# Performance work log

Hardware: AMD Instinct MI355X
Metric: run time of the kernel (lower is better)

Reference implementation:

```python
import jax, jax.numpy as jnp
import numpy as np

N, I, R, A, O, HEADS, HW, KS = 16, 128, 256, 256, 256, 8, 24, 3
HC = A // HEADS  # head channels
DN = ('NCHW', 'OIHW', 'NCHW')


def _conv(x, w, padding):
    return jax.lax.conv_general_dilated(x, w, (1, 1), padding, dimension_numbers=DN)


def setup_inputs() -> dict:
    key = jax.random.key(0)
    ks = jax.random.split(key, 16)
    g = lambda k, shape, fan: jax.random.normal(k, shape, jnp.float32) * (fan ** -0.5)
    return {
        'x': jax.random.normal(ks[0], (N, I, HW, HW), jnp.float32),
        'h0': jax.random.normal(ks[1], (N, R, HW, HW), jnp.float32) * 0.1,
        'c0': jax.random.normal(ks[2], (N, R, HW, HW), jnp.float32) * 0.1,
        'w_in': g(ks[3], (R, I, 1, 1), I),
        'b_in': jnp.zeros((R,), jnp.float32),
        'wq_x': g(ks[4], (A, R, KS, KS), R * KS * KS * 2 * HC),
        'wq_h': g(ks[5], (A, R, KS, KS), R * KS * KS * 2 * HC),
        'wk_x': g(ks[6], (A, R, KS, KS), R * KS * KS),
        'wk_h': g(ks[7], (A, R, KS, KS), R * KS * KS),
        'wv_x': g(ks[8], (A, R, KS, KS), R * KS * KS * 2),
        'wv_h': g(ks[9], (A, R, KS, KS), R * KS * KS * 2),
        'bv': jnp.zeros((A,), jnp.float32),
        'wg_a': g(ks[10], (4 * R, A, 1, 1), A * 3),
        'bg': jnp.zeros((4 * R,), jnp.float32),
        'wg_x': g(ks[11], (4 * R, R, KS, KS), R * KS * KS * 3),
        'wg_h': g(ks[12], (4 * R, R, KS, KS), R * KS * KS * 3),
        'w_out': g(ks[13], (O, R, 1, 1), R),
        'b_out': jnp.zeros((O,), jnp.float32),
    }


def reference(x, h0, c0, w_in, b_in, wq_x, wq_h, wk_x, wk_h, wv_x, wv_h, bv,
              wg_a, bg, wg_x, wg_h, w_out, b_out):
    # input accumulation (1x1 conv per input, summed; single input here)
    xin = _conv(x, w_in, 'VALID') + b_in[None, :, None, None]  # [N,R,H,W]
    # q: SAME-padded 3x3 convs of x and h (Accumulate = sum)
    q = _conv(xin, wq_x, 'SAME') + _conv(h0, wq_h, 'SAME')      # [N,A,H,W]
    # k, v: VALID 3x3 convs -> spatially reduced key/value positions
    k = _conv(xin, wk_x, 'VALID') + _conv(h0, wk_h, 'VALID')    # [N,A,H-2,W-2]
    v = _conv(xin, wv_x, 'VALID') + _conv(h0, wv_h, 'VALID') + bv[None, :, None, None]
    Q = HW * HW
    D = (HW - KS + 1) * (HW - KS + 1)
    qh = q.reshape(N, HEADS, HC, Q)
    kh = k.reshape(N, HEADS, HC, D)
    vh = v.reshape(N, HEADS, HC, D)
    w = jax.nn.softmax(jnp.einsum('ngcq,ngcd->ngqd', qh, kh), axis=-1)  # [N,G,Q,D]
    a = jnp.einsum('ngcd,ngqd->ngcq', vh, w).reshape(N, A, HW, HW)
    # fused i,f,g,o gate projections: 1x1 conv on a + 3x3 SAME convs on x and h
    gates = (_conv(a, wg_a, 'VALID') + bg[None, :, None, None]
             + _conv(xin, wg_x, 'SAME') + _conv(h0, wg_h, 'SAME'))      # [N,4R,H,W]
    i, f, gg, o = jnp.split(gates, 4, axis=1)
    c = jax.nn.sigmoid(f) * c0 + jax.nn.sigmoid(i) * jnp.tanh(gg)
    h = jax.nn.sigmoid(o) * jnp.tanh(c)
    return _conv(h, w_out, 'VALID') + b_out[None, :, None, None]
```

## Files before the change

### kernel.cpp

```cpp
#include <hip/hip_runtime.h>
#include <cstddef>

constexpr int kN  = 16;
constexpr int kI  = 128;
constexpr int kHW = 24;
constexpr int kQ  = 576;
constexpr int kD  = 484;
constexpr int kDP = 512;
constexpr int kPP = 676;

constexpr int kKT1 = 144;
constexpr int kKT2 = 8;
constexpr int kKT3 = 8;

constexpr size_t H_XPAD   = 0;
constexpr size_t H_HPAD   = 2768896;
constexpr size_t H_APACK1 = 5537792;
constexpr size_t H_APACK2 = 13795328;
constexpr size_t H_APACK3 = 14057472;
constexpr size_t H_A16    = 14123008;
constexpr size_t H_H16    = 16482304;
constexpr size_t H_Q16C   = 18841600;
constexpr size_t H_KT16   = 21200896;
constexpr size_t H_VC16   = 23298048;
constexpr size_t HALF_ELEMS = 25395200;
constexpr size_t HALF_BYTES = HALF_ELEMS * 2;
constexpr size_t F_G = 0;

using half4    = __attribute__((ext_vector_type(4))) _Float16;
using half8    = __attribute__((ext_vector_type(8))) _Float16;
using floatx16 = __attribute__((ext_vector_type(16))) float;

__device__ __forceinline__ float sigm(float x) { return 1.0f / (1.0f + __expf(-x)); }
__device__ __forceinline__ float tanh_f(float x) {
    float e = __expf(2.0f * fabsf(x));
    float r = 1.0f - 2.0f / (e + 1.0f);
    return copysignf(r, x);
}

__device__ __forceinline__ half8 LD8(const _Float16* p) { return *(const half8*)p; }
__device__ __forceinline__ void ST8(_Float16* p, half8 v) { *(half8*)p = v; }

__global__ void pack1_kernel(const float* __restrict__ wq_x, const float* __restrict__ wq_h,
                             const float* __restrict__ wk_x, const float* __restrict__ wk_h,
                             const float* __restrict__ wv_x, const float* __restrict__ wv_h,
                             const float* __restrict__ wg_x, const float* __restrict__ wg_h,
                             _Float16* __restrict__ dst) {
    int pidx = blockIdx.x * 256 + threadIdx.x;
    int j = pidx & 7, row = (pidx >> 3) & 127, hl = (pidx >> 10) & 1, kk = (pidx >> 11) & 1;
    int tile = pidx >> 12;
    int mt = tile / kKT1, kt = tile - mt * kKT1;
    int m = mt * 128 + row;
    int k = kt * 32 + kk * 16 + hl * 8 + j;
    int srcs = (k >= 2304) ? 1 : 0;
    int r = k - srcs * 2304;
    int tap = r >> 8, ic = r & 255;
    const float *s1, *s2; int mm;
    if (m < 256)      { s1 = wq_x; s2 = wq_h; mm = m; }
    else if (m < 512) { s1 = wk_x; s2 = wk_h; mm = m - 256; }
    else if (m < 768) { s1 = wv_x; s2 = wv_h; mm = m - 512; }
    else              { s1 = wg_x; s2 = wg_h; mm = m - 768; }
    const float* sp = srcs ? s2 : s1;
    dst[pidx] = (_Float16)sp[(size_t)mm * 2304 + ic * 9 + tap];
}

__global__ void pack_flat_kernel(const float* __restrict__ src, _Float16* __restrict__ dst,
                                 int Ktot, int Ktiles) {
    int pidx = blockIdx.x * 256 + threadIdx.x;
    int j = pidx & 7, row = (pidx >> 3) & 127, hl = (pidx >> 10) & 1, kk = (pidx >> 11) & 1;
    int tile = pidx >> 12;
    int mt = tile / Ktiles, kt = tile - mt * Ktiles;
    int m = mt * 128 + row;
    int k = kt * 32 + kk * 16 + hl * 8 + j;
    dst[pidx] = (_Float16)src[(size_t)m * Ktot + k];
}

__global__ void pad_nhwc_kernel(const float* __restrict__ src, _Float16* __restrict__ dst) {
    __shared__ float tile[32][65];
    int pxt = blockIdx.x, ict = blockIdx.y, n = blockIdx.z;
    int tid = threadIdx.x;
    {
        int icl = tid >> 6, pxl = tid & 63;
        #pragma unroll
        for (int rep = 0; rep < 8; ++rep) {
            int ic = ict * 32 + rep * 4 + icl;
            tile[rep * 4 + icl][pxl] = src[((size_t)n * 256 + ic) * kQ + pxt * 64 + pxl];
        }
    }
    __syncthreads();
    {
        int icl = tid & 31, pxl0 = tid >> 5;
        #pragma unroll
        for (int rep = 0; rep < 8; ++rep) {
            int pxl = rep * 8 + pxl0;
            int px = pxt * 64 + pxl;
            int y = px / kHW, x = px - y * kHW;
            dst[((size_t)n * kPP + (size_t)(y + 1) * 26 + (x + 1)) * 256 + ict * 32 + icl] =
                (_Float16)tile[icl][pxl];
        }
    }
}

__global__ void conv1x1_pad_kernel(const float* __restrict__ x, const float* __restrict__ w,
                                   const float* __restrict__ b, _Float16* __restrict__ out) {
    int px = blockIdx.x * 64 + threadIdx.x;
    int n = blockIdx.z;
    int oc0 = __builtin_amdgcn_readfirstlane(blockIdx.y * 16 + threadIdx.y * 4);
    const float* ip = x + (size_t)n * kI * kQ + px;
    float acc[4] = {0.f, 0.f, 0.f, 0.f};
    #pragma unroll 4
    for (int ic = 0; ic < kI; ++ic) {
        float xv = ip[(size_t)ic * kQ];
        #pragma unroll
        for (int j = 0; j < 4; ++j) acc[j] = fmaf(xv, w[(size_t)(oc0 + j) * kI + ic], acc[j]);
    }
    int y = px / kHW, xc = px - y * kHW;
    _Float16* op = out + ((size_t)n * kPP + (size_t)(y + 1) * 26 + (xc + 1)) * 256 + oc0;
    #pragma unroll
    for (int j = 0; j < 4; ++j) op[j] = (_Float16)(acc[j] + b[oc0 + j]);
}

template<int BMODE, int EMODE>
__global__ __launch_bounds__(256)
void gemm_kernel(const _Float16* __restrict__ Apack,
                 const _Float16* __restrict__ B1, const _Float16* __restrict__ B2,
                 _Float16* __restrict__ q16, _Float16* __restrict__ k16,
                 _Float16* __restrict__ v16, float* __restrict__ pf,
                 const float* __restrict__ bias, int Ktiles, int Ktot) {
    __shared__ _Float16 Bs[2][2048];
    const int tid = threadIdx.x;
    const int wv = tid >> 6, lane = tid & 63, l31 = lane & 31, hl = lane >> 5;
    const int mt = blockIdx.x, nt = blockIdx.y, n = blockIdx.z;

    floatx16 acc0 = {};
    floatx16 acc1 = {};

    const _Float16* aptr = Apack + (size_t)mt * Ktiles * 4096
                         + (size_t)hl * 1024 + (size_t)(wv * 32 + l31) * 8;

    const int px_l = tid >> 2, bc = tid & 3;
    const int px = nt * 64 + px_l;
    const int by = px / kHW, bx = px - by * kHW;

    const int wofs = px_l * 32 + ((bc ^ ((px_l >> 1) & 3)) << 3);
    const int sw = (l31 >> 1) & 3;
    const int r00 = l31 * 32        + ((hl ^ sw) << 3);
    const int r01 = (32 + l31) * 32 + ((hl ^ sw) << 3);
    const int r10 = l31 * 32        + (((2 + hl) ^ sw) << 3);
    const int r11 = (32 + l31) * 32 + (((2 + hl) ^ sw) << 3);

    for (int kt = 0; kt < Ktiles; ++kt) {
        const _Float16* bp;
        if (BMODE == 0) {
            int srcs = (kt >= 72) ? 1 : 0;
            int t2 = kt - srcs * 72;
            int tap = t2 >> 3, ict = t2 & 7;
            int ty = (tap * 11) >> 5;
            int tx = tap - ty * 3;
            const _Float16* img = srcs ? B2 : B1;
            bp = img + ((size_t)n * kPP + (size_t)(by + ty) * 26 + (bx + tx)) * 256
                     + ict * 32 + bc * 8;
        } else {
            bp = B1 + ((size_t)n * kQ + px) * Ktot + kt * 32 + bc * 8;
        }
        half8 bv = LD8(bp);
        half8 a0 = LD8(aptr);
        half8 a1 = LD8(aptr + 2048);
        aptr += 4096;
        ST8(&Bs[kt & 1][wofs], bv);
        __syncthreads();
        const _Float16* bb = Bs[kt & 1];
        half8 b00 = LD8(bb + r00);
        half8 b01 = LD8(bb + r01);
        half8 b10 = LD8(bb + r10);
        half8 b11 = LD8(bb + r11);
        acc0 = __builtin_amdgcn_mfma_f32_32x32x16_f16(a0, b00, acc0, 0, 0, 0);
        acc1 = __builtin_amdgcn_mfma_f32_32x32x16_f16(a0, b01, acc1, 0, 0, 0);
        acc0 = __builtin_amdgcn_mfma_f32_32x32x16_f16(a1, b10, acc0, 0, 0, 0);
        acc1 = __builtin_amdgcn_mfma_f32_32x32x16_f16(a1, b11, acc1, 0, 0, 0);
    }

    const int mbase = mt * 128 + wv * 32;
    #pragma unroll
    for (int t2 = 0; t2 < 2; ++t2) {
        const floatx16& A = t2 ? acc1 : acc0;
        int pxe = nt * 64 + t2 * 32 + l31;
        #pragma unroll
        for (int r = 0; r < 16; ++r) {
            int rowi = (r & 3) + 8 * (r >> 2) + 4 * hl;
            int m = mbase + rowi;
            float val = A[r];
            if (EMODE == 0) {
                if (m < 256) {
                    q16[((size_t)n * 256 + m) * kQ + pxe] = (_Float16)val;
                } else if (m < 768) {
                    int ch = m & 255;
                    int yy = pxe / kHW, xx = pxe - yy * kHW;
                    if (yy >= 1 && yy <= 22 && xx >= 1 && xx <= 22) {
                        int d = (yy - 1) * 22 + (xx - 1);
                        int head = n * 8 + (ch >> 5);
                        if (m < 512)
                            k16[((size_t)head * kDP + d) * 32 + (ch & 31)] = (_Float16)val;
                        else
                            v16[((size_t)head * 32 + (ch & 31)) * kDP + d] = (_Float16)(val + bias[ch]);
                    }
                } else {
                    pf[((size_t)n * 1024 + (m - 768)) * kQ + pxe] = val;
                }
            } else if (EMODE == 1) {
                size_t o = ((size_t)n * 1024 + m) * kQ + pxe;
                pf[o] = val + pf[o] + bias[m];
            } else {
                pf[((size_t)n * 256 + m) * kQ + pxe] = val + bias[m];
            }
        }
    }
}

__global__ __launch_bounds__(128)
void attn_kernel(const _Float16* __restrict__ q16c, const _Float16* __restrict__ kT16,
                 const _Float16* __restrict__ vC16, _Float16* __restrict__ a16) {
    const int lane = threadIdx.x & 63;
    const int wv   = threadIdx.x >> 6;
    const int l31 = lane & 31, hl = lane >> 5;
    const int head = blockIdx.y;
    const int n = head >> 3, hd = head & 7;
    const int qt = blockIdx.x * 2 + wv;
    const int q0 = qt * 32;

    half8 qf0, qf1;
    {
        const _Float16* qb = q16c + ((size_t)n * 256 + hd * 32 + hl * 8) * kQ + q0 + l31;
        #pragma unroll
        for (int j = 0; j < 8; ++j) {
            qf0[j] = qb[(size_t)j * kQ];
            qf1[j] = qb[(size_t)(16 + j) * kQ];
        }
    }

    const _Float16* kbase0 = kT16 + ((size_t)head * kDP + l31) * 32 + hl * 8;
    const _Float16* vbase0 = vC16 + ((size_t)head * 32 + l31) * kDP + hl * 8;

    floatx16 acc = {};
    float m_run = -1e30f, l_run = 0.f;

    half8 kf0 = LD8(kbase0);
    half8 kf1 = LD8(kbase0 + 16);

    for (int dt = 0; dt < 16; ++dt) {
        const int d0 = dt * 32;
        floatx16 S = {};
        S = __builtin_amdgcn_mfma_f32_32x32x16_f16(kf0, qf0, S, 0, 0, 0);
        S = __builtin_amdgcn_mfma_f32_32x32x16_f16(kf1, qf1, S, 0, 0, 0);

        half8 vf0 = LD8(vbase0 + d0);
        half8 vf1 = LD8(vbase0 + d0 + 16);
        if (dt < 15) {
            kf0 = LD8(kbase0 + (size_t)(d0 + 32) * 32);
            kf1 = LD8(kbase0 + (size_t)(d0 + 32) * 32 + 16);
        }

        if (dt == 15) {
            #pragma unroll
            for (int r = 0; r < 16; ++r)
                if (!(hl == 0 && r < 4)) S[r] = -1e30f;
        }

        float tmax = S[0];
        #pragma unroll
        for (int r = 1; r < 16; ++r) tmax = fmaxf(tmax, S[r]);
        tmax = fmaxf(tmax, __shfl_xor(tmax, 32));
        float mnew = fmaxf(m_run, tmax);
        float f = __expf(m_run - mnew);
        float p[16], psum = 0.f;
        #pragma unroll
        for (int r = 0; r < 16; ++r) { p[r] = __expf(S[r] - mnew); psum += p[r]; }
        psum += __shfl_xor(psum, 32);
        l_run = f * l_run + psum;
        #pragma unroll
        for (int r = 0; r < 16; ++r) acc[r] *= f;
        m_run = mnew;

        float other[16];
        #pragma unroll
        for (int r = 0; r < 16; ++r) other[r] = __shfl_xor(p[r], 32);
        half8 pf0, pf1;
        #pragma unroll
        for (int t = 0; t < 4; ++t) {
            pf0[t]     = (_Float16)(hl ? other[4 + t]  : p[t]);
            pf0[4 + t] = (_Float16)(hl ? p[4 + t]      : other[t]);
            pf1[t]     = (_Float16)(hl ? other[12 + t] : p[8 + t]);
            pf1[4 + t] = (_Float16)(hl ? p[12 + t]     : other[8 + t]);
        }

        acc = __builtin_amdgcn_mfma_f32_32x32x16_f16(vf0, pf0, acc, 0, 0, 0);
        acc = __builtin_amdgcn_mfma_f32_32x32x16_f16(vf1, pf1, acc, 0, 0, 0);
    }

    float inv = 1.f / l_run;
    _Float16* ap = a16 + ((size_t)n * kQ + q0 + l31) * 256 + hd * 32;
    #pragma unroll
    for (int r = 0; r < 16; ++r) {
        int c = (r & 3) + 8 * (r >> 2) + 4 * hl;
        ap[c] = (_Float16)(acc[r] * inv);
    }
}

__global__ void lstm_kernel(const float* __restrict__ gates, const float* __restrict__ c0,
                            _Float16* __restrict__ h16) {
    int px = blockIdx.x * 64 + threadIdx.x;
    int r = blockIdx.y * 4 + threadIdx.y;
    int n = blockIdx.z;
    size_t base = (size_t)n * 1024 * kQ + px;
    float iv = gates[base + (size_t)r * kQ];
    float fv = gates[base + (size_t)(256 + r) * kQ];
    float gv = gates[base + (size_t)(512 + r) * kQ];
    float ov = gates[base + (size_t)(768 + r) * kQ];
    float c = sigm(fv) * c0[((size_t)n * 256 + r) * kQ + px] + sigm(iv) * tanh_f(gv);
    float h = sigm(ov) * tanh_f(c);
    h16[((size_t)n * kQ + px) * 256 + r] = (_Float16)h;
}

extern "C" void kernel_launch(void* const* d_in, const int* in_sizes, int n_in,
                              void* d_out, int out_size, void* d_ws, size_t ws_size,
                              hipStream_t stream) {
    (void)in_sizes; (void)n_in; (void)out_size; (void)ws_size;
    const float* x     = (const float*)d_in[0];
    const float* h0    = (const float*)d_in[1];
    const float* c0    = (const float*)d_in[2];
    const float* w_in  = (const float*)d_in[3];
    const float* b_in  = (const float*)d_in[4];
    const float* wq_x  = (const float*)d_in[5];
    const float* wq_h  = (const float*)d_in[6];
    const float* wk_x  = (const float*)d_in[7];
    const float* wk_h  = (const float*)d_in[8];
    const float* wv_x  = (const float*)d_in[9];
    const float* wv_h  = (const float*)d_in[10];
    const float* bv    = (const float*)d_in[11];
    const float* wg_a  = (const float*)d_in[12];
    const float* bg    = (const float*)d_in[13];
    const float* wg_x  = (const float*)d_in[14];
    const float* wg_h  = (const float*)d_in[15];
    const float* w_out = (const float*)d_in[16];
    const float* b_out = (const float*)d_in[17];

    _Float16* wh = (_Float16*)d_ws;
    _Float16* xpad16  = wh + H_XPAD;
    _Float16* hpad16  = wh + H_HPAD;
    _Float16* apack1  = wh + H_APACK1;
    _Float16* apack2  = wh + H_APACK2;
    _Float16* apack3  = wh + H_APACK3;
    _Float16* a16     = wh + H_A16;
    _Float16* h16     = wh + H_H16;
    _Float16* q16c    = wh + H_Q16C;
    _Float16* kT16    = wh + H_KT16;
    _Float16* vC16    = wh + H_VC16;
    float* gbuf = (float*)((char*)d_ws + HALF_BYTES) + F_G;

    hipMemsetAsync(wh, 0, 11075584, stream);

    pack1_kernel<<<32256, 256, 0, stream>>>(wq_x, wq_h, wk_x, wk_h, wv_x, wv_h, wg_x, wg_h, apack1);
    pack_flat_kernel<<<1024, 256, 0, stream>>>(wg_a, apack2, 256, kKT2);
    pack_flat_kernel<<<256, 256, 0, stream>>>(w_out, apack3, 256, kKT3);

    pad_nhwc_kernel<<<dim3(9, 8, kN), 256, 0, stream>>>(h0, hpad16);
    conv1x1_pad_kernel<<<dim3(9, 16, kN), dim3(64, 4), 0, stream>>>(x, w_in, b_in, xpad16);

    gemm_kernel<0, 0><<<dim3(14, 9, kN), 256, 0, stream>>>(
        apack1, xpad16, hpad16, q16c, kT16, vC16, gbuf, bv, kKT1, 0);

    attn_kernel<<<dim3(9, 128), 128, 0, stream>>>(q16c, kT16, vC16, a16);

    gemm_kernel<1, 1><<<dim3(8, 9, kN), 256, 0, stream>>>(
        apack2, a16, nullptr, nullptr, nullptr, nullptr, gbuf, bg, kKT2, 256);

    lstm_kernel<<<dim3(9, 64, kN), dim3(64, 4), 0, stream>>>(gbuf, c0, h16);

    gemm_kernel<1, 2><<<dim3(2, 9, kN), 256, 0, stream>>>(
        apack3, h16, nullptr, nullptr, nullptr, nullptr, (float*)d_out, b_out, kKT3, 256);
}
```

Baseline: 457.3 us.

## Fuse gate convolutions, attention projection and LSTM cell into one GEMM epilogue

```diff
diff --git a/kernel.cpp b/kernel.cpp
--- a/kernel.cpp
+++ b/kernel.cpp
@@ -9,25 +9,21 @@
 constexpr int kDP = 512;
 constexpr int kPP = 676;
 
-constexpr int kKT1 = 144;
-constexpr int kKT2 = 8;
-constexpr int kKT3 = 8;
+constexpr int kKTQKV = 144;
+constexpr int kKTG   = 152;
+constexpr int kKTO   = 8;
 
 constexpr size_t H_XPAD   = 0;
 constexpr size_t H_HPAD   = 2768896;
-constexpr size_t H_APACK1 = 5537792;
-constexpr size_t H_APACK2 = 13795328;
-constexpr size_t H_APACK3 = 14057472;
+constexpr size_t H_APQKV  = 5537792;
+constexpr size_t H_APG    = 9076736;
+constexpr size_t H_APO    = 14057472;
 constexpr size_t H_A16    = 14123008;
 constexpr size_t H_H16    = 16482304;
 constexpr size_t H_Q16C   = 18841600;
 constexpr size_t H_KT16   = 21200896;
 constexpr size_t H_VC16   = 23298048;
-constexpr size_t HALF_ELEMS = 25395200;
-constexpr size_t HALF_BYTES = HALF_ELEMS * 2;
-constexpr size_t F_G = 0;
-
-using half4    = __attribute__((ext_vector_type(4))) _Float16;
+
 using half8    = __attribute__((ext_vector_type(8))) _Float16;
 using floatx16 = __attribute__((ext_vector_type(16))) float;
 
@@ -37,42 +33,58 @@
     float r = 1.0f - 2.0f / (e + 1.0f);
     return copysignf(r, x);
 }
-
 __device__ __forceinline__ half8 LD8(const _Float16* p) { return *(const half8*)p; }
 __device__ __forceinline__ void ST8(_Float16* p, half8 v) { *(half8*)p = v; }
 
-__global__ void pack1_kernel(const float* __restrict__ wq_x, const float* __restrict__ wq_h,
-                             const float* __restrict__ wk_x, const float* __restrict__ wk_h,
-                             const float* __restrict__ wv_x, const float* __restrict__ wv_h,
-                             const float* __restrict__ wg_x, const float* __restrict__ wg_h,
-                             _Float16* __restrict__ dst) {
+
+__global__ void pack_qkv_kernel(const float* __restrict__ wq_x, const float* __restrict__ wq_h,
+                                const float* __restrict__ wk_x, const float* __restrict__ wk_h,
+                                const float* __restrict__ wv_x, const float* __restrict__ wv_h,
+                                _Float16* __restrict__ dst) {
     int pidx = blockIdx.x * 256 + threadIdx.x;
-    int j = pidx & 7, row = (pidx >> 3) & 127, hl = (pidx >> 10) & 1, kk = (pidx >> 11) & 1;
-    int tile = pidx >> 12;
-    int mt = tile / kKT1, kt = tile - mt * kKT1;
-    int m = mt * 128 + row;
+    int j = pidx & 7, row = (pidx >> 3) & 255, hl = (pidx >> 11) & 1, kk = (pidx >> 12) & 1;
+    int tile = pidx >> 13;
+    int mb = tile / kKTQKV, kt = tile - mb * kKTQKV;
     int k = kt * 32 + kk * 16 + hl * 8 + j;
     int srcs = (k >= 2304) ? 1 : 0;
     int r = k - srcs * 2304;
     int tap = r >> 8, ic = r & 255;
-    const float *s1, *s2; int mm;
-    if (m < 256)      { s1 = wq_x; s2 = wq_h; mm = m; }
-    else if (m < 512) { s1 = wk_x; s2 = wk_h; mm = m - 256; }
-    else if (m < 768) { s1 = wv_x; s2 = wv_h; mm = m - 512; }
-    else              { s1 = wg_x; s2 = wg_h; mm = m - 768; }
-    const float* sp = srcs ? s2 : s1;
-    dst[pidx] = (_Float16)sp[(size_t)mm * 2304 + ic * 9 + tap];
-}
-
-__global__ void pack_flat_kernel(const float* __restrict__ src, _Float16* __restrict__ dst,
-                                 int Ktot, int Ktiles) {
+    const float* w;
+    if (mb == 0)      w = srcs ? wq_h : wq_x;
+    else if (mb == 1) w = srcs ? wk_h : wk_x;
+    else              w = srcs ? wv_h : wv_x;
+    dst[pidx] = (_Float16)w[((size_t)row * 256 + ic) * 9 + tap];
+}
+
+__global__ void pack_gates_kernel(const float* __restrict__ wg_x, const float* __restrict__ wg_h,
+                                  const float* __restrict__ wg_a, _Float16* __restrict__ dst) {
     int pidx = blockIdx.x * 256 + threadIdx.x;
-    int j = pidx & 7, row = (pidx >> 3) & 127, hl = (pidx >> 10) & 1, kk = (pidx >> 11) & 1;
-    int tile = pidx >> 12;
-    int mt = tile / Ktiles, kt = tile - mt * Ktiles;
-    int m = mt * 128 + row;
+    int j = pidx & 7, row = (pidx >> 3) & 255, hl = (pidx >> 11) & 1, kk = (pidx >> 12) & 1;
+    int tile = pidx >> 13;
+    int mb = tile / kKTG, kt = tile - mb * kKTG;
+    int P = mb * 256 + row;
+    int T = P >> 5, ch_local = (P >> 2) & 7, g = P & 3;
+    int m = g * 256 + T * 8 + ch_local;
     int k = kt * 32 + kk * 16 + hl * 8 + j;
-    dst[pidx] = (_Float16)src[(size_t)m * Ktot + k];
+    float val;
+    if (k < 4608) {
+        int srcs = (k >= 2304) ? 1 : 0;
+        int r = k - srcs * 2304;
+        int tap = r >> 8, ic = r & 255;
+        const float* w = srcs ? wg_h : wg_x;
+        val = w[((size_t)m * 256 + ic) * 9 + tap];
+    } else {
+        val = wg_a[(size_t)m * 256 + (k - 4608)];
+    }
+    dst[pidx] = (_Float16)val;
+}
+
+__global__ void pack_out_kernel(const float* __restrict__ src, _Float16* __restrict__ dst) {
+    int pidx = blockIdx.x * 256 + threadIdx.x;
+    int j = pidx & 7, row = (pidx >> 3) & 255, hl = (pidx >> 11) & 1, kk = (pidx >> 12) & 1;
+    int kt = pidx >> 13;
+    int k = kt * 32 + kk * 16 + hl * 8 + j;
+    dst[pidx] = (_Float16)src[(size_t)row * 256 + k];
 }
 
 __global__ void pad_nhwc_kernel(const float* __restrict__ src, _Float16* __restrict__ dst) {
@@ -124,34 +136,35 @@
 __global__ __launch_bounds__(256)
 void gemm_kernel(const _Float16* __restrict__ Apack,
                  const _Float16* __restrict__ B1, const _Float16* __restrict__ B2,
+                 const _Float16* __restrict__ B3,
                  _Float16* __restrict__ q16, _Float16* __restrict__ k16,
-                 _Float16* __restrict__ v16, float* __restrict__ pf,
+                 _Float16* __restrict__ v16, _Float16* __restrict__ h16,
+                 const float* __restrict__ c0, float* __restrict__ outf,
                  const float* __restrict__ bias, int Ktiles, int Ktot) {
     __shared__ _Float16 Bs[2][2048];
     const int tid = threadIdx.x;
     const int wv = tid >> 6, lane = tid & 63, l31 = lane & 31, hl = lane >> 5;
-    const int mt = blockIdx.x, nt = blockIdx.y, n = blockIdx.z;
-
-    floatx16 acc0 = {};
-    floatx16 acc1 = {};
-
-    const _Float16* aptr = Apack + (size_t)mt * Ktiles * 4096
-                         + (size_t)hl * 1024 + (size_t)(wv * 32 + l31) * 8;
+    const int nt = blockIdx.x, mb = blockIdx.y, n = blockIdx.z;
+
+    floatx16 acc00 = {}, acc01 = {}, acc10 = {}, acc11 = {};
+
+    const _Float16* aK0 = Apack + (size_t)mb * Ktiles * 8192
+                        + hl * 2048 + (size_t)(wv * 64 + l31) * 8;
+    const _Float16* aK1 = aK0 + 4096;
 
     const int px_l = tid >> 2, bc = tid & 3;
     const int px = nt * 64 + px_l;
     const int by = px / kHW, bx = px - by * kHW;
-
-    const int wofs = px_l * 32 + ((bc ^ ((px_l >> 1) & 3)) << 3);
-    const int sw = (l31 >> 1) & 3;
-    const int r00 = l31 * 32        + ((hl ^ sw) << 3);
-    const int r01 = (32 + l31) * 32 + ((hl ^ sw) << 3);
-    const int r10 = l31 * 32        + (((2 + hl) ^ sw) << 3);
-    const int r11 = (32 + l31) * 32 + (((2 + hl) ^ sw) << 3);
+    const int wofs = px_l * 32 + ((bc ^ (px_l & 3)) << 3);
+    const int sw = l31 & 3;
+    const int r00 = l31 * 32 + ((hl ^ sw) << 3);
+    const int r10 = l31 * 32 + (((2 + hl) ^ sw) << 3);
 
     for (int kt = 0; kt < Ktiles; ++kt) {
         const _Float16* bp;
-        if (BMODE == 0) {
+        if (BMODE == 2 && kt >= 144) {
+            bp = B3 + ((size_t)n * kQ + px) * 256 + (kt - 144) * 32 + bc * 8;
+        } else if (BMODE == 0 || BMODE == 2) {
             int srcs = (kt >= 72) ? 1 : 0;
             int t2 = kt - srcs * 72;
             int tap = t2 >> 3, ict = t2 & 7;
@@ -163,55 +176,79 @@
         } else {
             bp = B1 + ((size_t)n * kQ + px) * Ktot + kt * 32 + bc * 8;
         }
-        half8 bv = LD8(bp);
-        half8 a0 = LD8(aptr);
-        half8 a1 = LD8(aptr + 2048);
-        aptr += 4096;
+        half8 bv  = LD8(bp);
+        half8 a00 = LD8(aK0);
+        half8 a0m = LD8(aK0 + 256);
+        half8 a10 = LD8(aK1);
+        half8 a1m = LD8(aK1 + 256);
+        aK0 += 8192; aK1 += 8192;
         ST8(&Bs[kt & 1][wofs], bv);
         __syncthreads();
         const _Float16* bb = Bs[kt & 1];
         half8 b00 = LD8(bb + r00);
-        half8 b01 = LD8(bb + r01);
+        half8 b01 = LD8(bb + r00 + 1024);
         half8 b10 = LD8(bb + r10);
-        half8 b11 = LD8(bb + r11);
-        acc0 = __builtin_amdgcn_mfma_f32_32x32x16_f16(a0, b00, acc0, 0, 0, 0);
-        acc1 = __builtin_amdgcn_mfma_f32_32x32x16_f16(a0, b01, acc1, 0, 0, 0);
-        acc0 = __builtin_amdgcn_mfma_f32_32x32x16_f16(a1, b10, acc0, 0, 0, 0);
-        acc1 = __builtin_amdgcn_mfma_f32_32x32x16_f16(a1, b11, acc1, 0, 0, 0);
-    }
-
-    const int mbase = mt * 128 + wv * 32;
+        half8 b11 = LD8(bb + r10 + 1024);
+        acc00 = __builtin_amdgcn_mfma_f32_32x32x16_f16(a00, b00, acc00, 0, 0, 0);
+        acc01 = __builtin_amdgcn_mfma_f32_32x32x16_f16(a00, b01, acc01, 0, 0, 0);
+        acc10 = __builtin_amdgcn_mfma_f32_32x32x16_f16(a0m, b00, acc10, 0, 0, 0);
+        acc11 = __builtin_amdgcn_mfma_f32_32x32x16_f16(a0m, b01, acc11, 0, 0, 0);
+        acc00 = __builtin_amdgcn_mfma_f32_32x32x16_f16(a10, b10, acc00, 0, 0, 0);
+        acc01 = __builtin_amdgcn_mfma_f32_32x32x16_f16(a10, b11, acc01, 0, 0, 0);
+        acc10 = __builtin_amdgcn_mfma_f32_32x32x16_f16(a1m, b10, acc10, 0, 0, 0);
+        acc11 = __builtin_amdgcn_mfma_f32_32x32x16_f16(a1m, b11, acc11, 0, 0, 0);
+    }
+
     #pragma unroll
-    for (int t2 = 0; t2 < 2; ++t2) {
-        const floatx16& A = t2 ? acc1 : acc0;
-        int pxe = nt * 64 + t2 * 32 + l31;
-        #pragma unroll
-        for (int r = 0; r < 16; ++r) {
-            int rowi = (r & 3) + 8 * (r >> 2) + 4 * hl;
-            int m = mbase + rowi;
-            float val = A[r];
+    for (int mtile = 0; mtile < 2; ++mtile) {
+        #pragma unroll
+        for (int ntile = 0; ntile < 2; ++ntile) {
+            const floatx16& A = mtile ? (ntile ? acc11 : acc10) : (ntile ? acc01 : acc00);
+            const int pxe = nt * 64 + ntile * 32 + l31;
             if (EMODE == 0) {
-                if (m < 256) {
-                    q16[((size_t)n * 256 + m) * kQ + pxe] = (_Float16)val;
-                } else if (m < 768) {
-                    int ch = m & 255;
+                const int mrow = wv * 64 + mtile * 32;
+                if (mb == 0) {
+                    #pragma unroll
+                    for (int r = 0; r < 16; ++r) {
+                        int rowi = (r & 3) + 8 * (r >> 2) + 4 * hl;
+                        q16[((size_t)n * 256 + mrow + rowi) * kQ + pxe] = (_Float16)A[r];
+                    }
+                } else {
                     int yy = pxe / kHW, xx = pxe - yy * kHW;
                     if (yy >= 1 && yy <= 22 && xx >= 1 && xx <= 22) {
                         int d = (yy - 1) * 22 + (xx - 1);
-                        int head = n * 8 + (ch >> 5);
-                        if (m < 512)
-                            k16[((size_t)head * kDP + d) * 32 + (ch & 31)] = (_Float16)val;
-                        else
-                            v16[((size_t)head * 32 + (ch & 31)) * kDP + d] = (_Float16)(val + bias[ch]);
+                        #pragma unroll
+                        for (int r = 0; r < 16; ++r) {
+                            int ch = mrow + (r & 3) + 8 * (r >> 2) + 4 * hl;
+                            int head = n * 8 + (ch >> 5);
+                            if (mb == 1)
+                                k16[((size_t)head * kDP + d) * 32 + (ch & 31)] = (_Float16)A[r];
+                            else
+                                v16[((size_t)head * 32 + (ch & 31)) * kDP + d] =
+                                    (_Float16)(A[r] + bias[ch]);
+                        }
                     }
-                } else {
-                    pf[((size_t)n * 1024 + (m - 768)) * kQ + pxe] = val;
                 }
-            } else if (EMODE == 1) {
-                size_t o = ((size_t)n * 1024 + m) * kQ + pxe;
-                pf[o] = val + pf[o] + bias[m];
+            } else if (EMODE == 3) {
+                const int T = mb * 8 + wv * 2 + mtile;
+                #pragma unroll
+                for (int q4 = 0; q4 < 4; ++q4) {
+                    int c = T * 8 + 2 * q4 + hl;
+                    float iv = A[4 * q4 + 0] + bias[c];
+                    float fv = A[4 * q4 + 1] + bias[256 + c];
+                    float gv = A[4 * q4 + 2] + bias[512 + c];
+                    float ov = A[4 * q4 + 3] + bias[768 + c];
+                    float c0v = c0[((size_t)n * 256 + c) * kQ + pxe];
+                    float cn = sigm(fv) * c0v + sigm(iv) * tanh_f(gv);
+                    h16[((size_t)n * kQ + pxe) * 256 + c] = (_Float16)(sigm(ov) * tanh_f(cn));
+                }
             } else {
-                pf[((size_t)n * 256 + m) * kQ + pxe] = val + bias[m];
+                const int mrow = wv * 64 + mtile * 32;
+                #pragma unroll
+                for (int r = 0; r < 16; ++r) {
+                    int m = mrow + (r & 3) + 8 * (r >> 2) + 4 * hl;
+                    outf[((size_t)n * 256 + m) * kQ + pxe] = A[r] + bias[m];
+                }
             }
         }
     }
@@ -304,21 +341,6 @@
         int c = (r & 3) + 8 * (r >> 2) + 4 * hl;
         ap[c] = (_Float16)(acc[r] * inv);
     }
-}
-
-__global__ void lstm_kernel(const float* __restrict__ gates, const float* __restrict__ c0,
-                            _Float16* __restrict__ h16) {
-    int px = blockIdx.x * 64 + threadIdx.x;
-    int r = blockIdx.y * 4 + threadIdx.y;
-    int n = blockIdx.z;
-    size_t base = (size_t)n * 1024 * kQ + px;
-    float iv = gates[base + (size_t)r * kQ];
-    float fv = gates[base + (size_t)(256 + r) * kQ];
-    float gv = gates[base + (size_t)(512 + r) * kQ];
-    float ov = gates[base + (size_t)(768 + r) * kQ];
-    float c = sigm(fv) * c0[((size_t)n * 256 + r) * kQ + px] + sigm(iv) * tanh_f(gv);
-    float h = sigm(ov) * tanh_f(c);
-    h16[((size_t)n * kQ + px) * 256 + r] = (_Float16)h;
 }
 
 extern "C" void kernel_launch(void* const* d_in, const int* in_sizes, int n_in,
@@ -347,35 +369,35 @@
     _Float16* wh = (_Float16*)d_ws;
     _Float16* xpad16  = wh + H_XPAD;
     _Float16* hpad16  = wh + H_HPAD;
-    _Float16* apack1  = wh + H_APACK1;
-    _Float16* apack2  = wh + H_APACK2;
-    _Float16* apack3  = wh + H_APACK3;
+    _Float16* apqkv   = wh + H_APQKV;
+    _Float16* apg     = wh + H_APG;
+    _Float16* apo     = wh + H_APO;
     _Float16* a16     = wh + H_A16;
     _Float16* h16     = wh + H_H16;
     _Float16* q16c    = wh + H_Q16C;
     _Float16* kT16    = wh + H_KT16;
     _Float16* vC16    = wh + H_VC16;
-    float* gbuf = (float*)((char*)d_ws + HALF_BYTES) + F_G;
 
     hipMemsetAsync(wh, 0, 11075584, stream);
 
-    pack1_kernel<<<32256, 256, 0, stream>>>(wq_x, wq_h, wk_x, wk_h, wv_x, wv_h, wg_x, wg_h, apack1);
-    pack_flat_kernel<<<1024, 256, 0, stream>>>(wg_a, apack2, 256, kKT2);
-    pack_flat_kernel<<<256, 256, 0, stream>>>(w_out, apack3, 256, kKT3);
+    pack_qkv_kernel<<<13824, 256, 0, stream>>>(wq_x, wq_h, wk_x, wk_h, wv_x, wv_h, apqkv);
+    pack_gates_kernel<<<19456, 256, 0, stream>>>(wg_x, wg_h, wg_a, apg);
+    pack_out_kernel<<<256, 256, 0, stream>>>(w_out, apo);
 
     pad_nhwc_kernel<<<dim3(9, 8, kN), 256, 0, stream>>>(h0, hpad16);
     conv1x1_pad_kernel<<<dim3(9, 16, kN), dim3(64, 4), 0, stream>>>(x, w_in, b_in, xpad16);
 
-    gemm_kernel<0, 0><<<dim3(14, 9, kN), 256, 0, stream>>>(
-        apack1, xpad16, hpad16, q16c, kT16, vC16, gbuf, bv, kKT1, 0);
+    gemm_kernel<0, 0><<<dim3(9, 3, kN), 256, 0, stream>>>(
+        apqkv, xpad16, hpad16, nullptr, q16c, kT16, vC16, nullptr,
+        nullptr, nullptr, bv, kKTQKV, 0);
 
     attn_kernel<<<dim3(9, 128), 128, 0, stream>>>(q16c, kT16, vC16, a16);
 
-    gemm_kernel<1, 1><<<dim3(8, 9, kN), 256, 0, stream>>>(
-        apack2, a16, nullptr, nullptr, nullptr, nullptr, gbuf, bg, kKT2, 256);
-
-    lstm_kernel<<<dim3(9, 64, kN), dim3(64, 4), 0, stream>>>(gbuf, c0, h16);
-
-    gemm_kernel<1, 2><<<dim3(2, 9, kN), 256, 0, stream>>>(
-        apack3, h16, nullptr, nullptr, nullptr, nullptr, (float*)d_out, b_out, kKT3, 256);
-}
+    gemm_kernel<2, 3><<<dim3(9, 4, kN), 256, 0, stream>>>(
+        apg, xpad16, hpad16, a16, nullptr, nullptr, nullptr, h16,
+        c0, nullptr, bg, kKTG, 0);
+
+    gemm_kernel<1, 2><<<dim3(9, 1, kN), 256, 0, stream>>>(
+        apo, h16, nullptr, nullptr, nullptr, nullptr, nullptr, nullptr,
+        nullptr, (float*)d_out, b_out, kKTO, 256);
+}
```

Measured after the change: 526.2 us. +15.1%, slower.
